# Performance work log

Measured on AMD Instinct MI355X. Metric: run time of the kernel, lower is better.

The kernel has to match this reference:

```python
import jax, jax.numpy as jnp
import numpy as np

N, E = 50000, 800000
F_IN, F_OUT, H, F_EDGE = 256, 32, 8, 5
LEAKY_SLOPE = 0.2


def setup_inputs() -> dict:
    key = jax.random.key(0)
    ks = jax.random.split(key, 6)
    x = jax.random.normal(ks[0], (N, F_IN), dtype=jnp.float32)
    edge_index = jax.random.randint(ks[1], (2, E), 0, N, dtype=jnp.int64)
    edge_attr = jax.random.normal(ks[2], (E, F_EDGE), dtype=jnp.float32)
    degree_src = jax.random.randint(ks[3], (E,), 0, 64, dtype=jnp.int64)
    # Xavier-uniform params
    lim_W = float(np.sqrt(6.0 / (F_IN + F_OUT)))
    W = jax.random.uniform(ks[4], (H, F_IN, F_OUT), minval=-lim_W, maxval=lim_W, dtype=jnp.float32)
    A = 2 * F_OUT + F_EDGE
    lim_a = float(np.sqrt(6.0 / (H + A)))
    a = jax.random.uniform(ks[5], (H, A), minval=-lim_a, maxval=lim_a, dtype=jnp.float32)
    lim_e = float(np.sqrt(1.0 / F_EDGE))
    W_edge_w = jax.random.uniform(jax.random.fold_in(key, 7), (F_EDGE, F_EDGE), minval=-lim_e, maxval=lim_e, dtype=jnp.float32)
    return {"x": x, "edge_index": edge_index, "edge_attr": edge_attr,
            "degree_src": degree_src, "W": W, "a": a, "W_edge_w": W_edge_w}


def reference(x, edge_index, edge_attr, degree_src, W, a, W_edge_w):
    n = x.shape[0]
    h, f_out = W.shape[0], W.shape[2]
    src, dst = edge_index[0], edge_index[1]
    # per-head projection: (N, H, F_out)
    Wh = jnp.einsum('nf,hfo->nho', x, W)
    # split attention vector instead of materializing the concat
    a_src, a_dst, a_e = a[:, :f_out], a[:, f_out:2 * f_out], a[:, 2 * f_out:]
    ef = edge_attr @ W_edge_w.T                      # (E, F_edge)
    e = (jnp.einsum('eho,ho->eh', Wh[src], a_src)
         + jnp.einsum('eho,ho->eh', Wh[dst], a_dst)
         + ef @ a_e.T)                                # (E, H)
    e = jax.nn.leaky_relu(e, LEAKY_SLOPE)
    scale = 1.0 / jnp.sqrt(jnp.clip(degree_src.astype(jnp.float32), 1.0, None))
    e = e * scale[:, None]
    # segment softmax over src; torch scatter_reduce amax include_self=True with zeros init -> max includes 0
    e_max = jnp.maximum(jax.ops.segment_max(e, src, num_segments=n), 0.0)
    e_exp = jnp.exp(e - e_max[src])
    e_sum = jax.ops.segment_sum(e_exp, src, num_segments=n)
    alpha = e_exp / (e_sum[src] + 1e-16)             # (E, H)
    msg = Wh[dst] * alpha[:, :, None]                # (E, H, F_out)
    out = jax.ops.segment_sum(msg, src, num_segments=n)
    out = jax.nn.elu(out.reshape(n, h * f_out))
    return out, alpha
```

## Files before the change

### kernel.cpp

```cpp
#include <hip/hip_runtime.h>
#include <hip/hip_bf16.h>
#include <math.h>

#define NN 50000
#define NE 800000
#define FIN 256
#define FOUT 32
#define NH 8
#define FE 5
#define AROW 69

typedef float f32x4 __attribute__((ext_vector_type(4)));
typedef short bf16x8 __attribute__((ext_vector_type(8)));

static __device__ __forceinline__ unsigned short f2bf(float f) {
    unsigned u = __float_as_uint(f);
    unsigned r = (u + 0x7FFFu + ((u >> 16) & 1u)) >> 16;
    return (unsigned short)r;
}
static __device__ __forceinline__ float bf2f(unsigned short b) {
    return __uint_as_float(((unsigned)b) << 16);
}

__global__ __launch_bounds__(256) void k_prep(const float* __restrict__ W,
                                              const float* __restrict__ a,
                                              const float* __restrict__ Wew,
                                              float* __restrict__ C,
                                              unsigned short* __restrict__ Bh,
                                              unsigned short* __restrict__ Bl,
                                              unsigned short* __restrict__ Bsh,
                                              unsigned short* __restrict__ Bsl) {
    int t = threadIdx.x;
    if (blockIdx.x == 0) {
        if (t < NH * FE) {
            int h = t / FE, k = t % FE;
            float s = 0.f;
            for (int j = 0; j < FE; ++j) s += a[h * AROW + 2 * FOUT + j] * Wew[j * FE + k];
            C[t] = s;
        }
        int k = t;
        for (int h = 0; h < NH; ++h) {
            float s1v = 0.f, s2v = 0.f;
            for (int o = 0; o < FOUT; ++o) {
                float wv = W[(size_t)h * (FIN * FOUT) + (size_t)k * FOUT + o];
                s1v += wv * a[h * AROW + o];
                s2v += wv * a[h * AROW + FOUT + o];
            }
            unsigned short h1 = f2bf(s1v);
            Bsh[h * 256 + k] = h1;
            Bsl[h * 256 + k] = f2bf(s1v - bf2f(h1));
            unsigned short h2 = f2bf(s2v);
            Bsh[(8 + h) * 256 + k] = h2;
            Bsl[(8 + h) * 256 + k] = f2bf(s2v - bf2f(h2));
        }
    } else {
        int c = blockIdx.x - 1;
        int k = t;
        int h = c >> 5, o = c & 31;
        float f = W[(size_t)h * (FIN * FOUT) + (size_t)k * FOUT + o];
        unsigned short hi = f2bf(f);
        unsigned short lo = f2bf(f - bf2f(hi));
        Bh[c * 256 + k] = hi;
        Bl[c * 256 + k] = lo;
    }
}

__global__ __launch_bounds__(256) void k_gemm_mfma(const float* __restrict__ x,
                                                   const unsigned short* __restrict__ Bh,
                                                   const unsigned short* __restrict__ Bl,
                                                   const unsigned short* __restrict__ Bsh,
                                                   const unsigned short* __restrict__ Bsl,
                                                   unsigned short* __restrict__ Whb,
                                                   float* __restrict__ s1,
                                                   float* __restrict__ s2,
                                                   const int* __restrict__ ei,
                                                   int* __restrict__ counts, int nrows) {
    __shared__ __align__(16) unsigned short Ah[64 * 56];
    int t = threadIdx.x;
    int w = t >> 6, l = t & 63;
    int r = l & 15, blk = l >> 4;
    int row0 = blockIdx.x * 64;
    int c0 = w * 64;

    f32x4 acc[4][4];
    f32x4 acc_s = (f32x4)(0.f);
#pragma unroll
    for (int i = 0; i < 4; ++i)
#pragma unroll
        for (int j = 0; j < 4; ++j) acc[i][j] = (f32x4)(0.f);

    int srow = t >> 2, skq = (t & 3) * 8;
    const size_t xrow = (size_t)(row0 + srow) * FIN;

    for (int k0 = 0; k0 < FIN; k0 += 32) {
        {
            float v[8];
            if (row0 + srow < nrows) {
                f32x4 u0 = *(const f32x4*)&x[xrow + k0 + skq];
                f32x4 u1 = *(const f32x4*)&x[xrow + k0 + skq + 4];
                v[0] = u0.x; v[1] = u0.y; v[2] = u0.z; v[3] = u0.w;
                v[4] = u1.x; v[5] = u1.y; v[6] = u1.z; v[7] = u1.w;
            } else {
#pragma unroll
                for (int e = 0; e < 8; ++e) v[e] = 0.f;
            }
            bf16x8 hi;
#pragma unroll
            for (int e = 0; e < 8; ++e) hi[e] = (short)f2bf(v[e]);
            *(bf16x8*)&Ah[srow * 56 + skq] = hi;
        }
        __syncthreads();
        bf16x8 ah[4];
#pragma unroll
        for (int rt = 0; rt < 4; ++rt)
            ah[rt] = *(const bf16x8*)&Ah[(rt * 16 + r) * 56 + blk * 8];
#pragma unroll
        for (int ct = 0; ct < 4; ++ct) {
            int c = c0 + ct * 16 + r;
            bf16x8 bh = *(const bf16x8*)&Bh[c * 256 + k0 + blk * 8];
            bf16x8 bl = *(const bf16x8*)&Bl[c * 256 + k0 + blk * 8];
#pragma unroll
            for (int rt = 0; rt < 4; ++rt) {
                acc[rt][ct] = __builtin_amdgcn_mfma_f32_16x16x32_bf16(ah[rt], bh, acc[rt][ct], 0, 0, 0);
                acc[rt][ct] = __builtin_amdgcn_mfma_f32_16x16x32_bf16(ah[rt], bl, acc[rt][ct], 0, 0, 0);
            }
        }
        {
            bf16x8 bsh = *(const bf16x8*)&Bsh[r * 256 + k0 + blk * 8];
            bf16x8 bsl = *(const bf16x8*)&Bsl[r * 256 + k0 + blk * 8];
            acc_s = __builtin_amdgcn_mfma_f32_16x16x32_bf16(ah[w], bsh, acc_s, 0, 0, 0);
            acc_s = __builtin_amdgcn_mfma_f32_16x16x32_bf16(ah[w], bsl, acc_s, 0, 0, 0);
        }
        __syncthreads();
    }

#pragma unroll
    for (int rt = 0; rt < 4; ++rt) {
#pragma unroll
        for (int reg = 0; reg < 4; ++reg) {
            int row = row0 + rt * 16 + blk * 4 + reg;
            if (row < nrows) {
#pragma unroll
                for (int ct = 0; ct < 4; ++ct)
                    Whb[(size_t)row * 256 + c0 + ct * 16 + r] = f2bf(acc[rt][ct][reg]);
            }
        }
    }
#pragma unroll
    for (int reg = 0; reg < 4; ++reg) {
        int row = row0 + w * 16 + blk * 4 + reg;
        if (row < nrows) {
            if (r < 8) s1[row * NH + r] = acc_s[reg];
            else       s2[row * NH + (r - 8)] = acc_s[reg];
        }
    }
    int e0 = (blockIdx.x * 256 + t) * 4;
    if (e0 + 3 < NE) {
        int4 e4 = *(const int4*)&ei[e0];
        atomicAdd(&counts[e4.x], 1);
        atomicAdd(&counts[e4.y], 1);
        atomicAdd(&counts[e4.z], 1);
        atomicAdd(&counts[e4.w], 1);
    } else {
        for (int q = 0; q < 4; ++q)
            if (e0 + q < NE) atomicAdd(&counts[ei[e0 + q]], 1);
    }
}

__global__ __launch_bounds__(256) void k_scanA(const int* __restrict__ counts,
                                               int* __restrict__ part,
                                               int* __restrict__ bsums, int n) {
    __shared__ int lds[256];
    int t = threadIdx.x;
    int base = blockIdx.x * 1024;
    int i0 = base + t * 4;
    int v0 = (i0 + 0 < n) ? counts[i0 + 0] : 0;
    int v1 = (i0 + 1 < n) ? counts[i0 + 1] : 0;
    int v2 = (i0 + 2 < n) ? counts[i0 + 2] : 0;
    int v3 = (i0 + 3 < n) ? counts[i0 + 3] : 0;
    int l0 = v0, l1 = l0 + v1, l2 = l1 + v2, l3 = l2 + v3;
    lds[t] = l3;
    __syncthreads();
    for (int off = 1; off < 256; off <<= 1) {
        int val = lds[t];
        if (t >= off) val += lds[t - off];
        __syncthreads();
        lds[t] = val;
        __syncthreads();
    }
    int excl = (t == 0) ? 0 : lds[t - 1];
    if (i0 + 0 < n) part[i0 + 0] = excl;
    if (i0 + 1 < n) part[i0 + 1] = excl + l0;
    if (i0 + 2 < n) part[i0 + 2] = excl + l1;
    if (i0 + 3 < n) part[i0 + 3] = excl + l2;
    if (t == 255) bsums[blockIdx.x] = lds[255];
}

__global__ void k_scanB(const int* __restrict__ bsums, int* __restrict__ boffs, int nb) {
    __shared__ int s[64];
    int t = threadIdx.x;
    int v = (t < nb) ? bsums[t] : 0;
    s[t] = v;
    __syncthreads();
    for (int off = 1; off < 64; off <<= 1) {
        int x = s[t];
        if (t >= off) x += s[t - off];
        __syncthreads();
        s[t] = x;
        __syncthreads();
    }
    if (t < nb) boffs[t] = s[t] - v;
}

__global__ __launch_bounds__(256) void k_scanC(int* __restrict__ row_ptr,
                                               const int* __restrict__ boffs, int n, int total) {
    int i = blockIdx.x * 256 + threadIdx.x;
    if (i < n) row_ptr[i] += boffs[i >> 10];
    else if (i == n) row_ptr[n] = total;
}

__global__ __launch_bounds__(256) void k_scatlog(const int* __restrict__ ei,
                                                 const float* __restrict__ eattr,
                                                 const int* __restrict__ degs,
                                                 const float* __restrict__ s1,
                                                 const float* __restrict__ s2,
                                                 const float* __restrict__ C,
                                                 const int* __restrict__ row_ptr,
                                                 int* __restrict__ counts,
                                                 unsigned short* __restrict__ e_perm,
                                                 int2* __restrict__ de_perm) {
    __shared__ float Cl[NH * FE];
    int t = threadIdx.x;
    if (t < NH * FE) Cl[t] = C[t];
    __syncthreads();
    int e = blockIdx.x * 256 + t;
    if (e >= NE) return;
    int src = ei[e], dst = ei[NE + e];
    int dg = degs[e];
    float scale = rsqrtf((float)(dg > 1 ? dg : 1));
    float ea0 = eattr[(size_t)e * FE + 0];
    float ea1 = eattr[(size_t)e * FE + 1];
    float ea2 = eattr[(size_t)e * FE + 2];
    float ea3 = eattr[(size_t)e * FE + 3];
    float ea4 = eattr[(size_t)e * FE + 4];
    float4 s1a = *(const float4*)&s1[src * NH];
    float4 s1b = *(const float4*)&s1[src * NH + 4];
    float4 s2a = *(const float4*)&s2[dst * NH];
    float4 s2b = *(const float4*)&s2[dst * NH + 4];
    float vs1[8] = {s1a.x, s1a.y, s1a.z, s1a.w, s1b.x, s1b.y, s1b.z, s1b.w};
    float vs2[8] = {s2a.x, s2a.y, s2a.z, s2a.w, s2b.x, s2b.y, s2b.z, s2b.w};
    bf16x8 v;
#pragma unroll
    for (int h = 0; h < NH; ++h) {
        float q = vs1[h] + vs2[h] + ea0 * Cl[h * FE + 0] + ea1 * Cl[h * FE + 1] +
                  ea2 * Cl[h * FE + 2] + ea3 * Cl[h * FE + 3] + ea4 * Cl[h * FE + 4];
        q = q > 0.f ? q : 0.2f * q;
        v[h] = (short)f2bf(q * scale);
    }
    int old = atomicSub(&counts[src], 1);
    int p = row_ptr[src] + old - 1;
    *(bf16x8*)&e_perm[(size_t)p * 8] = v;
    de_perm[p] = make_int2(dst, e);
}

__global__ __launch_bounds__(256) void k_smmsg(const int* __restrict__ row_ptr,
                                               const unsigned short* __restrict__ e_perm,
                                               const int2* __restrict__ de_perm,
                                               const unsigned short* __restrict__ Whb,
                                               float* __restrict__ out_alpha,
                                               float* __restrict__ out) {
    __shared__ float al[4][256];
    __shared__ int dl[4][32];
    __shared__ int el[4][32];
    int t = threadIdx.x;
    int w = t >> 6, l = t & 63;
    int n = blockIdx.x * 4 + w;
    if (n >= NN) return;
    int start = row_ptr[n], deg = row_ptr[n + 1] - start;
    int j = l >> 3, h = l & 7;

    float vc[4];
#pragma unroll
    for (int q = 0; q < 4; ++q) {
        int b = j + 8 * q;
        vc[q] = (b < deg) ? bf2f(e_perm[(size_t)(start + b) * 8 + h]) : -1e30f;
    }
    float mx = 0.f;
#pragma unroll
    for (int q = 0; q < 4; ++q) mx = fmaxf(mx, vc[q]);
    for (int b = 32 + j; b < deg; b += 8)
        mx = fmaxf(mx, bf2f(e_perm[(size_t)(start + b) * 8 + h]));
    mx = fmaxf(mx, __shfl_xor(mx, 8));
    mx = fmaxf(mx, __shfl_xor(mx, 16));
    mx = fmaxf(mx, __shfl_xor(mx, 32));
    float m = mx;
    float ex[4];
    float sm = 0.f;
#pragma unroll
    for (int q = 0; q < 4; ++q) { ex[q] = __expf(vc[q] - m); sm += ex[q]; }
    for (int b = 32 + j; b < deg; b += 8)
        sm += __expf(bf2f(e_perm[(size_t)(start + b) * 8 + h]) - m);
    sm += __shfl_xor(sm, 8);
    sm += __shfl_xor(sm, 16);
    sm += __shfl_xor(sm, 32);
    float inv = 1.f / (sm + 1e-16f);
    f32x4 acc = (f32x4)(0.f);
    int hh = l >> 3;
    for (int base = 0; base < deg; base += 32) {
        int cnt = deg - base;
        if (cnt > 32) cnt = 32;
        if (l < cnt) {
            int2 de = de_perm[start + base + l];
            dl[w][l] = de.x;
            el[w][l] = de.y;
        }
        asm volatile("s_waitcnt lgkmcnt(0)" ::: "memory");
#pragma unroll
        for (int q = 0; q < 4; ++q) {
            int b = base + j + 8 * q;
            if (b < deg) {
                float av = (base == 0 ? ex[q]
                                      : __expf(bf2f(e_perm[(size_t)(start + b) * 8 + h]) - m)) * inv;
                al[w][(j + 8 * q) * 8 + h] = av;
                out_alpha[(size_t)el[w][j + 8 * q] * 8 + h] = av;
            }
        }
        asm volatile("s_waitcnt lgkmcnt(0)" ::: "memory");
        for (int jj = 0; jj < cnt; ++jj) {
            int d = dl[w][jj];
            float av = al[w][jj * 8 + hh];
            ushort4 u = *(const ushort4*)&Whb[(size_t)d * 256 + l * 4];
            acc.x += av * bf2f(u.x);
            acc.y += av * bf2f(u.y);
            acc.z += av * bf2f(u.z);
            acc.w += av * bf2f(u.w);
        }
        asm volatile("s_waitcnt lgkmcnt(0)" ::: "memory");
    }
    f32x4 o;
    o.x = acc.x > 0.f ? acc.x : expm1f(acc.x);
    o.y = acc.y > 0.f ? acc.y : expm1f(acc.y);
    o.z = acc.z > 0.f ? acc.z : expm1f(acc.z);
    o.w = acc.w > 0.f ? acc.w : expm1f(acc.w);
    *(f32x4*)&out[(size_t)n * 256 + l * 4] = o;
}

extern "C" void kernel_launch(void* const* d_in, const int* in_sizes, int n_in,
                              void* d_out, int out_size, void* d_ws, size_t ws_size,
                              hipStream_t stream) {
    const float* x     = (const float*)d_in[0];
    const int*   ei    = (const int*)d_in[1];
    const float* eattr = (const float*)d_in[2];
    const int*   degs  = (const int*)d_in[3];
    const float* W     = (const float*)d_in[4];
    const float* a     = (const float*)d_in[5];
    const float* Wew   = (const float*)d_in[6];

    float* out       = (float*)d_out;
    float* out_alpha = out + (size_t)NN * 256;

    char* p = (char*)d_ws;
    auto alloc = [&](size_t bytes) -> char* {
        char* r = p;
        p += (bytes + 255) & ~(size_t)255;
        return r;
    };
    unsigned short* Whb     = (unsigned short*)alloc((size_t)NN * 256 * 2);
    float*          s1      = (float*)alloc((size_t)NN * NH * 4);
    float*          s2      = (float*)alloc((size_t)NN * NH * 4);
    float*          Cm      = (float*)alloc(NH * FE * 4);
    unsigned short* Bh      = (unsigned short*)alloc((size_t)256 * 256 * 2);
    unsigned short* Bl      = (unsigned short*)alloc((size_t)256 * 256 * 2);
    unsigned short* Bsh     = (unsigned short*)alloc((size_t)16 * 256 * 2);
    unsigned short* Bsl     = (unsigned short*)alloc((size_t)16 * 256 * 2);
    int*            counts  = (int*)alloc((size_t)NN * 4);
    int*            row_ptr = (int*)alloc((size_t)(NN + 1) * 4);
    int*            bsums   = (int*)alloc(64 * 4);
    int*            boffs   = (int*)alloc(64 * 4);
    unsigned short* e_perm  = (unsigned short*)alloc((size_t)NE * NH * 2);
    int2*           de_perm = (int2*)alloc((size_t)NE * 8);

    hipMemsetAsync(counts, 0, (size_t)NN * 4, stream);

    k_prep<<<257, 256, 0, stream>>>(W, a, Wew, Cm, Bh, Bl, Bsh, Bsl);
    k_gemm_mfma<<<(NN + 63) / 64, 256, 0, stream>>>(x, Bh, Bl, Bsh, Bsl, Whb, s1, s2,
                                                    ei, counts, NN);
    k_scanA<<<(NN + 1023) / 1024, 256, 0, stream>>>(counts, row_ptr, bsums, NN);
    k_scanB<<<1, 64, 0, stream>>>(bsums, boffs, (NN + 1023) / 1024);
    k_scanC<<<(NN + 1 + 255) / 256, 256, 0, stream>>>(row_ptr, boffs, NN, NE);
    k_scatlog<<<(NE + 255) / 256, 256, 0, stream>>>(ei, eattr, degs, s1, s2, Cm,
                                                    row_ptr, counts, e_perm, de_perm);
    k_smmsg<<<(NN + 3) / 4, 256, 0, stream>>>(row_ptr, e_perm, de_perm, Whb,
                                              out_alpha, out);
}
```

Before: 246.5 us.

## Double-buffer A tile and prefetch x and B fragments in projection GEMM

The projection GEMM now uses two LDS buffers for the bf16 A tile and drops the second barrier per k-step. It register-prefetches the next x slice while the current one is converted and consumed. The B and score-B fragments are also loaded before the barrier, so global latency overlaps with MFMA work. The cost is more registers, which may lower occupancy, and the full k-loop is unrolled.

```diff
diff --git a/kernel.cpp b/kernel.cpp
--- a/kernel.cpp
+++ b/kernel.cpp
@@ -75,7 +75,7 @@
                                                    float* __restrict__ s2,
                                                    const int* __restrict__ ei,
                                                    int* __restrict__ counts, int nrows) {
-    __shared__ __align__(16) unsigned short Ah[64 * 56];
+    __shared__ __align__(16) unsigned short Ah[2][64 * 56];
     int t = threadIdx.x;
     int w = t >> 6, l = t & 63;
     int r = l & 15, blk = l >> 4;
@@ -90,48 +90,51 @@
         for (int j = 0; j < 4; ++j) acc[i][j] = (f32x4)(0.f);
 
     int srow = t >> 2, skq = (t & 3) * 8;
-    const size_t xrow = (size_t)(row0 + srow) * FIN;
-
-    for (int k0 = 0; k0 < FIN; k0 += 32) {
+    bool arow_ok = (row0 + srow < nrows);
+    const float* xp = x + (size_t)(row0 + srow) * FIN + skq;
+
+    f32x4 xa0 = (f32x4)(0.f), xa1 = (f32x4)(0.f);
+    if (arow_ok) { xa0 = *(const f32x4*)xp; xa1 = *(const f32x4*)(xp + 4); }
+
+#pragma unroll
+    for (int ks = 0; ks < 8; ++ks) {
+        const int k0 = ks * 32;
         {
-            float v[8];
-            if (row0 + srow < nrows) {
-                f32x4 u0 = *(const f32x4*)&x[xrow + k0 + skq];
-                f32x4 u1 = *(const f32x4*)&x[xrow + k0 + skq + 4];
-                v[0] = u0.x; v[1] = u0.y; v[2] = u0.z; v[3] = u0.w;
-                v[4] = u1.x; v[5] = u1.y; v[6] = u1.z; v[7] = u1.w;
-            } else {
-#pragma unroll
-                for (int e = 0; e < 8; ++e) v[e] = 0.f;
-            }
             bf16x8 hi;
-#pragma unroll
-            for (int e = 0; e < 8; ++e) hi[e] = (short)f2bf(v[e]);
-            *(bf16x8*)&Ah[srow * 56 + skq] = hi;
-        }
-        __syncthreads();
-        bf16x8 ah[4];
-#pragma unroll
-        for (int rt = 0; rt < 4; ++rt)
-            ah[rt] = *(const bf16x8*)&Ah[(rt * 16 + r) * 56 + blk * 8];
+            hi[0] = (short)f2bf(xa0.x); hi[1] = (short)f2bf(xa0.y);
+            hi[2] = (short)f2bf(xa0.z); hi[3] = (short)f2bf(xa0.w);
+            hi[4] = (short)f2bf(xa1.x); hi[5] = (short)f2bf(xa1.y);
+            hi[6] = (short)f2bf(xa1.z); hi[7] = (short)f2bf(xa1.w);
+            *(bf16x8*)&Ah[ks & 1][srow * 56 + skq] = hi;
+        }
+        if (ks < 7 && arow_ok) {
+            xa0 = *(const f32x4*)(xp + (ks + 1) * 32);
+            xa1 = *(const f32x4*)(xp + (ks + 1) * 32 + 4);
+        }
+        bf16x8 bh[4], bl[4];
 #pragma unroll
         for (int ct = 0; ct < 4; ++ct) {
             int c = c0 + ct * 16 + r;
-            bf16x8 bh = *(const bf16x8*)&Bh[c * 256 + k0 + blk * 8];
-            bf16x8 bl = *(const bf16x8*)&Bl[c * 256 + k0 + blk * 8];
+            bh[ct] = *(const bf16x8*)&Bh[c * 256 + k0 + blk * 8];
+            bl[ct] = *(const bf16x8*)&Bl[c * 256 + k0 + blk * 8];
+        }
+        bf16x8 bsh = *(const bf16x8*)&Bsh[r * 256 + k0 + blk * 8];
+        bf16x8 bsl = *(const bf16x8*)&Bsl[r * 256 + k0 + blk * 8];
+        __syncthreads();
+        bf16x8 ah[4];
+#pragma unroll
+        for (int rt = 0; rt < 4; ++rt)
+            ah[rt] = *(const bf16x8*)&Ah[ks & 1][(rt * 16 + r) * 56 + blk * 8];
+#pragma unroll
+        for (int ct = 0; ct < 4; ++ct) {
 #pragma unroll
             for (int rt = 0; rt < 4; ++rt) {
-                acc[rt][ct] = __builtin_amdgcn_mfma_f32_16x16x32_bf16(ah[rt], bh, acc[rt][ct], 0, 0, 0);
-                acc[rt][ct] = __builtin_amdgcn_mfma_f32_16x16x32_bf16(ah[rt], bl, acc[rt][ct], 0, 0, 0);
+                acc[rt][ct] = __builtin_amdgcn_mfma_f32_16x16x32_bf16(ah[rt], bh[ct], acc[rt][ct], 0, 0, 0);
+                acc[rt][ct] = __builtin_amdgcn_mfma_f32_16x16x32_bf16(ah[rt], bl[ct], acc[rt][ct], 0, 0, 0);
             }
         }
-        {
-            bf16x8 bsh = *(const bf16x8*)&Bsh[r * 256 + k0 + blk * 8];
-            bf16x8 bsl = *(const bf16x8*)&Bsl[r * 256 + k0 + blk * 8];
-            acc_s = __builtin_amdgcn_mfma_f32_16x16x32_bf16(ah[w], bsh, acc_s, 0, 0, 0);
-            acc_s = __builtin_amdgcn_mfma_f32_16x16x32_bf16(ah[w], bsl, acc_s, 0, 0, 0);
-        }
-        __syncthreads();
+        acc_s = __builtin_amdgcn_mfma_f32_16x16x32_bf16(ah[w], bsh, acc_s, 0, 0, 0);
+        acc_s = __builtin_amdgcn_mfma_f32_16x16x32_bf16(ah[w], bsl, acc_s, 0, 0, 0);
     }
 
 #pragma unroll
```

Result: faster. 237.7 us (-3.6%).
